# Kernel tuning notes

Measured on AMD Instinct MI355X. Metric: run time of the kernel, lower is better.

The kernel has to match this reference:

```python
import jax, jax.numpy as jnp
import numpy as np

EPS = 1e-5
K_GROUP = 8  # k_group_size


def setup_inputs() -> dict:
    key = jax.random.key(0)
    ks = jax.random.split(key, 8)
    C = 384  # encoder_channel
    rn = lambda k, s: (jax.random.normal(k, s, dtype=jnp.float32) * 0.05)
    return {
        "point_groups": jax.random.normal(ks[0], (4, 256, 32, 3), dtype=jnp.float32),
        # first_conv: Conv1d(3,128,1)+BN+ReLU+Conv1d(128,256,1)
        "W1": rn(ks[1], (128, 3)), "b1": jnp.zeros(128, jnp.float32),
        "gamma1": jnp.ones(128, jnp.float32), "beta1": jnp.zeros(128, jnp.float32),
        "W2": rn(ks[2], (256, 128)), "b2": jnp.zeros(256, jnp.float32),
        # second_conv: Conv1d(512,512,1)+BN+ReLU+Conv1d(512,C,1)
        "W3": rn(ks[3], (512, 512)), "b3": jnp.zeros(512, jnp.float32),
        "gamma3": jnp.ones(512, jnp.float32), "beta3": jnp.zeros(512, jnp.float32),
        "W4": rn(ks[4], (C, 512)), "b4": jnp.zeros(C, jnp.float32),
        # K_Norm affine (out_dim = C, matching declared parameter shapes)
        "alpha": jnp.ones((1, 1, 1, C), jnp.float32),
        "beta_aff": jnp.zeros((1, 1, 1, C), jnp.float32),
        # fusion_layer: Conv1d(2C,C,1)+BN+ReLU
        "Wf": rn(ks[5], (C, 2 * C)), "bf": jnp.zeros(C, jnp.float32),
        "gammaf": jnp.ones(C, jnp.float32), "betaf": jnp.zeros(C, jnp.float32),
    }


def _conv1x1(x, W, b):  # x: (B,Cin,L), W: (Cout,Cin)
    return jnp.einsum("bcl,oc->bol", x, W) + b[None, :, None]


def _bn(x, gamma, beta):  # training-mode BatchNorm1d over (batch, length)
    mu = jnp.mean(x, axis=(0, 2), keepdims=True)
    var = jnp.var(x, axis=(0, 2), keepdims=True)
    xh = (x - mu) * jax.lax.rsqrt(var + EPS)
    return xh * gamma[None, :, None] + beta[None, :, None]


def reference(point_groups, W1, b1, gamma1, beta1, W2, b2, W3, b3, gamma3, beta3,
              W4, b4, alpha, beta_aff, Wf, bf, gammaf, betaf):
    bs, g, n, _ = point_groups.shape
    C = W4.shape[0]
    pg = point_groups.reshape(bs * g, n, 3)  # (B', n, 3)

    # first_conv stack
    f = _conv1x1(pg.transpose(0, 2, 1), W1, b1)           # (B',128,n)
    f = jax.nn.relu(_bn(f, gamma1, beta1))
    f = _conv1x1(f, W2, b2)                               # (B',256,n)
    fg = jnp.max(f, axis=2, keepdims=True)                # (B',256,1)
    f = jnp.concatenate([jnp.broadcast_to(fg, f.shape), f], axis=1)  # (B',512,n)

    # second_conv stack
    f = _conv1x1(f, W3, b3)
    f = jax.nn.relu(_bn(f, gamma3, beta3))
    f = _conv1x1(f, W4, b4)                               # (B',C,n)
    feat = f.transpose(0, 2, 1)                           # (B',n,C)

    # KNN within each group (self included, as in KNN(xyz,xyz))
    sq = jnp.sum(pg * pg, axis=-1)                        # (B',n)
    d = sq[:, :, None] + sq[:, None, :] - 2.0 * jnp.einsum("bnc,bmc->bnm", pg, pg)
    _, idx = jax.lax.top_k(-d, K_GROUP)                   # (B',n,K)

    gather = jax.vmap(lambda a, i: a[i])
    knn_x = gather(feat, idx)                             # (B',n,K,C)

    # K_Norm: center-relative normalization by global scalar std (torch.std, ddof=1)
    mean_x = feat[:, :, None, :]
    dx = knn_x - mean_x
    std_x = jnp.std(dx, ddof=1)
    knn_x = dx / (std_x + EPS)
    knn_x = alpha * knn_x + beta_aff                      # (B',n,K,C)

    enhanced = jnp.mean(knn_x, axis=2)                    # mean over K -> (B',n,C)
    enhanced = jnp.mean(enhanced, axis=1)                 # pool over n -> (B',C)

    fg2 = jnp.max(f, axis=2)                              # (B',C)
    fused_in = jnp.concatenate([fg2, enhanced], axis=1)[:, :, None]  # (B',2C,1)
    fused = jax.nn.relu(_bn(_conv1x1(fused_in, Wf, bf), gammaf, betaf))[:, :, 0]
    return fused.reshape(bs, g, C)
```

## Files before the change

kernel.cpp:

```cpp
#include <hip/hip_runtime.h>
#include <math.h>

#define EPS 1e-5f

typedef __attribute__((ext_vector_type(8))) short s16x8;
typedef __attribute__((ext_vector_type(4))) float f32x4;

__device__ __forceinline__ unsigned short f2bf(float x) {
    unsigned u = __float_as_uint(x);
    u += 0x7fffu + ((u >> 16) & 1u);
    return (unsigned short)(u >> 16);
}
__device__ __forceinline__ float bf2f(unsigned short h) {
    return __uint_as_float(((unsigned)h) << 16);
}
__device__ __forceinline__ unsigned long long pack4bf(float a, float b, float c, float d) {
    return (unsigned long long)f2bf(a)
         | ((unsigned long long)f2bf(b) << 16)
         | ((unsigned long long)f2bf(c) << 32)
         | ((unsigned long long)f2bf(d) << 48);
}

template<int CTRL>
__device__ __forceinline__ float dppmov(float x) {
    return __int_as_float(__builtin_amdgcn_update_dpp(
        0, __float_as_int(x), CTRL, 0xF, 0xF, true));
}
__device__ __forceinline__ float red16_sum(float x) {
    x += dppmov<0xB1>(x);
    x += dppmov<0x4E>(x);
    x += dppmov<0x141>(x);
    x += dppmov<0x140>(x);
    return x;
}
__device__ __forceinline__ float red16_max(float x) {
    x = fmaxf(x, dppmov<0xB1>(x));
    x = fmaxf(x, dppmov<0x4E>(x));
    x = fmaxf(x, dppmov<0x141>(x));
    x = fmaxf(x, dppmov<0x140>(x));
    return x;
}

__global__ __launch_bounds__(128) void k1_prep(
    const float* __restrict__ pg,
    const float* __restrict__ W2, const float* __restrict__ W3,
    const float* __restrict__ W4, const float* __restrict__ Wf,
    float* __restrict__ mom, int* __restrict__ idxw,
    unsigned short* __restrict__ W2b, unsigned short* __restrict__ W3b,
    unsigned short* __restrict__ W4b, unsigned short* __restrict__ Wfb,
    float* __restrict__ p3sb, float* __restrict__ p3qb)
{
    __shared__ float pgs[96];
    __shared__ float sqs[32];
    if (blockIdx.x >= 1024) {
        const int wb = blockIdx.x - 1024;
        const int i = wb * 128 + threadIdx.x;
        if (i < 32768)  W2b[i] = f2bf(W2[i]);
        if (i < 262144) W3b[i] = f2bf(W3[i]);
        if (i < 196608) W4b[i] = f2bf(W4[i]);
        if (i < 294912) Wfb[i] = f2bf(Wf[i]);
        if (wb < 16) {
            for (int j = threadIdx.x; j < 512; j += 128) {
                p3sb[wb*512 + j] = 0.f;
                p3qb[wb*512 + j] = 0.f;
            }
        }
        return;
    }
    const int b = blockIdx.x;
    const int t = threadIdx.x;
    if (t < 96) pgs[t] = pg[b * 96 + t];
    __syncthreads();
    if (t < 32) {
        float x = pgs[t*3+0], y = pgs[t*3+1], z = pgs[t*3+2];
        sqs[t] = x*x + y*y + z*z;
    }
    __syncthreads();
    if (t < 32) {
        const float x = pgs[t*3+0], y = pgs[t*3+1], z = pgs[t*3+2];
        float v[9] = {x, y, z, x*x, x*y, x*z, y*y, y*z, z*z};
        #pragma unroll
        for (int off = 16; off > 0; off >>= 1)
            #pragma unroll
            for (int j = 0; j < 9; ++j)
                v[j] += __shfl_down(v[j], off, 32);
        if (t == 0) {
            #pragma unroll
            for (int j = 0; j < 9; ++j)
                mom[j*1024 + b] = v[j];
        }
        const float sql = sqs[t];
        float dist[32];
        #pragma unroll
        for (int m = 0; m < 32; ++m) {
            float dot = x*pgs[m*3+0] + y*pgs[m*3+1] + z*pgs[m*3+2];
            dist[m] = sql + sqs[m] - 2.f*dot;
        }
        unsigned used = 0u;
        int* orow = idxw + b*256 + t*8;
        #pragma unroll
        for (int j = 0; j < 8; ++j) {
            float best = 3.4e38f; int bi = 0;
            #pragma unroll
            for (int m = 0; m < 32; ++m) {
                if (!((used >> m) & 1u) && dist[m] < best) { best = dist[m]; bi = m; }
            }
            used |= (1u << bi);
            orow[j] = bi;
        }
    }
}

__global__ __launch_bounds__(1024, 8) void k3_mfma(
    const float* __restrict__ pg,
    const float* __restrict__ W1, const float* __restrict__ b1,
    const float* __restrict__ gamma1, const float* __restrict__ beta1,
    const float* __restrict__ mom,
    const unsigned short* __restrict__ W2b, const float* __restrict__ b2,
    const unsigned short* __restrict__ W3b, const float* __restrict__ b3,
    unsigned short* __restrict__ h3b,
    float* __restrict__ p3sb, float* __restrict__ p3qb)
{
    const int g0 = blockIdx.x * 2;
    const int t = threadIdx.x;
    __shared__ __align__(16) unsigned short SB[26128];
    unsigned short* B1  = SB;
    unsigned short* F2  = SB + 8704;
    unsigned short* FGB = SB + 25600;
    __shared__ __align__(16) float sc1s[128], sh1s[128];
    __shared__ __align__(16) float W1s[384], b1s[128];
    __shared__ __align__(16) float pgs3[192];
    __shared__ float momS[9];

    if (t < 192) pgs3[t] = pg[g0*96 + t];
    if (t < 384) W1s[t] = W1[t];
    if (t < 128) b1s[t] = b1[t];
    {
        const int wv = t >> 6, ln = t & 63;
        if (wv < 9) {
            float s = 0.f;
            #pragma unroll
            for (int i = 0; i < 16; ++i)
                s += mom[wv*1024 + ln + 64*i];
            #pragma unroll
            for (int off = 32; off > 0; off >>= 1)
                s += __shfl_down(s, off, 64);
            if (ln == 0) momS[wv] = s;
        }
    }
    __syncthreads();

    if (t < 128) {
        const float Sx = momS[0], Sy = momS[1], Sz = momS[2];
        const float Sxx = momS[3], Sxy = momS[4], Sxz = momS[5];
        const float Syy = momS[6], Syz = momS[7], Szz = momS[8];
        const float w0 = W1s[t*3+0], w1 = W1s[t*3+1], w2 = W1s[t*3+2];
        const float bb = b1s[t];
        const float N = 32768.f;
        const float wd = w0*Sx + w1*Sy + w2*Sz;
        const float S = wd + N*bb;
        const float Q = w0*w0*Sxx + w1*w1*Syy + w2*w2*Szz
                      + 2.f*(w0*w1*Sxy + w0*w2*Sxz + w1*w2*Syz)
                      + 2.f*bb*wd + N*bb*bb;
        const float mu  = S * (1.f/32768.f);
        const float var = Q * (1.f/32768.f) - mu*mu;
        const float sc  = gamma1[t] * rsqrtf(var + EPS);
        sc1s[t] = sc;
        sh1s[t] = beta1[t] - mu * sc;
    }
    __syncthreads();

    {
        const int l = t >> 4, c0 = (t & 15) * 8;
        const float px = pgs3[l*3+0], py = pgs3[l*3+1], pz = pgs3[l*3+2];
        unsigned short ov[8];
        #pragma unroll
        for (int e = 0; e < 8; ++e) {
            const int c = c0 + e;
            float v = fmaf(W1s[c*3+2], pz, fmaf(W1s[c*3+1], py, fmaf(W1s[c*3+0], px, b1s[c])));
            float val = fmaxf(fmaf(v, sc1s[c], sh1s[c]), 0.f);
            ov[e] = f2bf(val);
        }
        uint4 o4;
        o4.x = (unsigned)ov[0] | ((unsigned)ov[1] << 16);
        o4.y = (unsigned)ov[2] | ((unsigned)ov[3] << 16);
        o4.z = (unsigned)ov[4] | ((unsigned)ov[5] << 16);
        o4.w = (unsigned)ov[6] | ((unsigned)ov[7] << 16);
        *(uint4*)&B1[l*136 + c0] = o4;
    }
    __syncthreads();

    const int wave = t >> 6;
    const int lane = t & 63;
    const int m    = lane & 15;
    const int quad = lane >> 4;

    f32x4 acc2[4];
    #pragma unroll
    for (int n = 0; n < 4; ++n)
        acc2[n] = (f32x4){0.f, 0.f, 0.f, 0.f};

    #pragma unroll
    for (int kt = 0; kt < 4; ++kt) {
        s16x8 bv[4];
        #pragma unroll
        for (int nt = 0; nt < 4; ++nt)
            bv[nt] = *(const s16x8*)&B1[(nt*16 + m)*136 + kt*32 + quad*8];
        s16x8 av = *(const s16x8*)(W2b + (size_t)(wave*16 + m)*128 + kt*32 + quad*8);
        #pragma unroll
        for (int nt = 0; nt < 4; ++nt)
            acc2[nt] = __builtin_amdgcn_mfma_f32_16x16x32_bf16(av, bv[nt], acc2[nt], 0, 0, 0);
    }

    {
        const int o0 = wave*16 + quad*4;
        #pragma unroll
        for (int r = 0; r < 4; ++r) {
            float bb = b2[o0 + r];
            #pragma unroll
            for (int nt = 0; nt < 4; ++nt) acc2[nt][r] += bb;
        }
        #pragma unroll
        for (int nt = 0; nt < 4; ++nt) {
            const int row = nt*16 + m;
            *(unsigned long long*)&F2[row*264 + o0] =
                pack4bf(acc2[nt][0], acc2[nt][1], acc2[nt][2], acc2[nt][3]);
        }
        float f0[4], f1[4];
        #pragma unroll
        for (int r = 0; r < 4; ++r) {
            f0[r] = red16_max(fmaxf(acc2[0][r], acc2[1][r]));
            f1[r] = red16_max(fmaxf(acc2[2][r], acc2[3][r]));
        }
        if (m == 0) {
            *(unsigned long long*)&FGB[o0]       = pack4bf(f0[0], f0[1], f0[2], f0[3]);
            *(unsigned long long*)&FGB[264 + o0] = pack4bf(f1[0], f1[1], f1[2], f1[3]);
        }
    }
    __syncthreads();

    unsigned short* dst = h3b + (size_t)blockIdx.x * 32768;
    const int binbase = (blockIdx.x & 15) * 512;
    #pragma unroll
    for (int mt = 0; mt < 2; ++mt) {
        const int ot = wave*2 + mt;
        const int o0 = ot*16 + quad*4;

        f32x4 facc = (f32x4){0.f, 0.f, 0.f, 0.f};
        #pragma unroll
        for (int kt = 0; kt < 8; ++kt) {
            s16x8 bg = *(const s16x8*)&FGB[(m & 1)*264 + kt*32 + quad*8];
            s16x8 av = *(const s16x8*)(W3b + (size_t)(ot*16 + m)*512 + kt*32 + quad*8);
            facc = __builtin_amdgcn_mfma_f32_16x16x32_bf16(av, bg, facc, 0, 0, 0);
        }

        f32x4 acc3[4];
        #pragma unroll
        for (int r = 0; r < 4; ++r) {
            float self = facc[r];
            float oth  = dppmov<0xB1>(self);
            float fg_g0 = (m & 1) ? oth : self;
            float fg_g1 = (m & 1) ? self : oth;
            float bb = b3[o0 + r];
            acc3[0][r] = bb + fg_g0;
            acc3[1][r] = bb + fg_g0;
            acc3[2][r] = bb + fg_g1;
            acc3[3][r] = bb + fg_g1;
        }

        #pragma unroll
        for (int kt = 0; kt < 8; ++kt) {
            s16x8 bv[4];
            #pragma unroll
            for (int nt = 0; nt < 4; ++nt)
                bv[nt] = *(const s16x8*)&F2[(nt*16 + m)*264 + kt*32 + quad*8];
            s16x8 av = *(const s16x8*)(W3b + (size_t)(ot*16 + m)*512 + 256 + kt*32 + quad*8);
            #pragma unroll
            for (int nt = 0; nt < 4; ++nt)
                acc3[nt] = __builtin_amdgcn_mfma_f32_16x16x32_bf16(av, bv[nt], acc3[nt], 0, 0, 0);
        }

        float s[4], q[4];
        #pragma unroll
        for (int r = 0; r < 4; ++r) {
            float x0 = acc3[0][r], x1 = acc3[1][r];
            float x2 = acc3[2][r], x3 = acc3[3][r];
            s[r] = (x0 + x1) + (x2 + x3);
            q[r] = (x0*x0 + x1*x1) + (x2*x2 + x3*x3);
        }
        {
            unsigned long long u0 = pack4bf(acc3[0][0], acc3[0][1], acc3[0][2], acc3[0][3]);
            unsigned long long u1 = pack4bf(acc3[1][0], acc3[1][1], acc3[1][2], acc3[1][3]);
            unsigned long long u2 = pack4bf(acc3[2][0], acc3[2][1], acc3[2][2], acc3[2][3]);
            unsigned long long u3 = pack4bf(acc3[3][0], acc3[3][1], acc3[3][2], acc3[3][3]);
            unsigned short* p = dst + (size_t)(ot*64 + lane) * 16;
            *(uint4*)(p)     = make_uint4((unsigned)u0, (unsigned)(u0 >> 32), (unsigned)u1, (unsigned)(u1 >> 32));
            *(uint4*)(p + 8) = make_uint4((unsigned)u2, (unsigned)(u2 >> 32), (unsigned)u3, (unsigned)(u3 >> 32));
        }
        #pragma unroll
        for (int r = 0; r < 4; ++r) {
            s[r] = red16_sum(s[r]);
            q[r] = red16_sum(q[r]);
        }
        if (m == 0) {
            #pragma unroll
            for (int r = 0; r < 4; ++r) {
                atomicAdd(&p3sb[binbase + o0 + r], s[r]);
                atomicAdd(&p3qb[binbase + o0 + r], q[r]);
            }
        }
    }
}

__global__ __launch_bounds__(768, 6) void k5_mfma(
    const unsigned short* __restrict__ h3b,
    const float* __restrict__ gamma3, const float* __restrict__ beta3,
    const float* __restrict__ p3sb, const float* __restrict__ p3qb,
    const unsigned short* __restrict__ W4b, const float* __restrict__ b4,
    const int* __restrict__ idxw,
    float* __restrict__ fg2, float* __restrict__ A,
    float* __restrict__ S1p, float* __restrict__ S2p)
{
    const int g0 = blockIdx.x * 2;
    const int t = threadIdx.x;
    __shared__ __align__(16) unsigned short SB[33280];
    unsigned short* B4 = SB;
    unsigned short* XT = SB;
    unsigned short* Mm = SB + 30720;
    __shared__ __align__(16) float sc3s[512], sh3s[512];
    __shared__ int icnt[2][32];
    __shared__ float r1[2][12], r2[2][12];

    if (t < 512) {
        float S = 0.f, Q = 0.f;
        #pragma unroll
        for (int bb = 0; bb < 16; ++bb) {
            S += p3sb[bb*512 + t];
            Q += p3qb[bb*512 + t];
        }
        float mu  = S * (1.f/32768.f);
        float var = Q * (1.f/32768.f) - mu*mu;
        float sc  = gamma3[t] * rsqrtf(var + EPS);
        sc3s[t] = sc;
        sh3s[t] = beta3[t] - mu * sc;
    }
    if (t < 64) icnt[t >> 5][t & 31] = 0;
    __syncthreads();

    {
        const uint4* src = (const uint4*)(h3b + (size_t)blockIdx.x * 32768);
        for (int i = t; i < 4096; i += 768) {
            uint4 hv = src[i];
            const int flat16 = i >> 1, half = i & 1;
            const int ln = flat16 & 63, m2 = ln & 15, q2 = ln >> 4;
            const int wm = flat16 >> 6;
            const int o0 = wm*16 + q2*4;
            const float4 sc = *(const float4*)&sc3s[o0];
            const float4 sh = *(const float4*)&sh3s[o0];
            const int rowa = (half*2)*16 + m2;
            float a0 = fmaxf(fmaf(bf2f((unsigned short)(hv.x       )), sc.x, sh.x), 0.f);
            float a1 = fmaxf(fmaf(bf2f((unsigned short)(hv.x >> 16 )), sc.y, sh.y), 0.f);
            float a2 = fmaxf(fmaf(bf2f((unsigned short)(hv.y       )), sc.z, sh.z), 0.f);
            float a3 = fmaxf(fmaf(bf2f((unsigned short)(hv.y >> 16 )), sc.w, sh.w), 0.f);
            float b0 = fmaxf(fmaf(bf2f((unsigned short)(hv.z       )), sc.x, sh.x), 0.f);
            float b1 = fmaxf(fmaf(bf2f((unsigned short)(hv.z >> 16 )), sc.y, sh.y), 0.f);
            float b2 = fmaxf(fmaf(bf2f((unsigned short)(hv.w       )), sc.z, sh.z), 0.f);
            float b3 = fmaxf(fmaf(bf2f((unsigned short)(hv.w >> 16 )), sc.w, sh.w), 0.f);
            *(unsigned long long*)&B4[rowa*520 + o0]        = pack4bf(a0, a1, a2, a3);
            *(unsigned long long*)&B4[(rowa + 16)*520 + o0] = pack4bf(b0, b1, b2, b3);
        }
    }
    __syncthreads();

    const int wave = t >> 6;
    const int lane = t & 63;
    const int m    = lane & 15;
    const int quad = lane >> 4;

    f32x4 acc4[2][4];
    #pragma unroll
    for (int mt = 0; mt < 2; ++mt)
        #pragma unroll
        for (int n = 0; n < 4; ++n)
            acc4[mt][n] = (f32x4){0.f, 0.f, 0.f, 0.f};

    #pragma unroll 4
    for (int kt = 0; kt < 16; ++kt) {
        s16x8 bv[4];
        #pragma unroll
        for (int nt = 0; nt < 4; ++nt)
            bv[nt] = *(const s16x8*)&B4[(nt*16 + m)*520 + kt*32 + quad*8];
        #pragma unroll
        for (int mt = 0; mt < 2; ++mt) {
            s16x8 av = *(const s16x8*)(W4b + (size_t)(wave*32 + mt*16 + m)*512 + kt*32 + quad*8);
            #pragma unroll
            for (int nt = 0; nt < 4; ++nt)
                acc4[mt][nt] = __builtin_amdgcn_mfma_f32_16x16x32_bf16(av, bv[nt], acc4[mt][nt], 0, 0, 0);
        }
    }

    #pragma unroll
    for (int mt = 0; mt < 2; ++mt) {
        const int o0 = wave*32 + mt*16 + quad*4;
        float f0[4], f1[4];
        #pragma unroll
        for (int r = 0; r < 4; ++r) {
            float bb = b4[o0 + r];
            #pragma unroll
            for (int nt = 0; nt < 4; ++nt) acc4[mt][nt][r] += bb;
            f0[r] = red16_max(fmaxf(acc4[mt][0][r], acc4[mt][1][r]));
            f1[r] = red16_max(fmaxf(acc4[mt][2][r], acc4[mt][3][r]));
        }
        if (m == 0) {
            #pragma unroll
            for (int r = 0; r < 4; ++r) {
                fg2[(size_t)g0*384 + o0 + r]     = f0[r];
                fg2[(size_t)(g0+1)*384 + o0 + r] = f1[r];
            }
        }
    }
    __syncthreads();

    #pragma unroll
    for (int mt = 0; mt < 2; ++mt) {
        const int o0 = wave*32 + mt*16 + quad*4;
        #pragma unroll
        for (int nt = 0; nt < 4; ++nt) {
            const int g = nt >> 1;
            const int l = (nt & 1)*16 + m;
            unsigned short* xg = XT + g*15360;
            #pragma unroll
            for (int r = 0; r < 4; ++r)
                xg[(o0 + r)*40 + l] = f2bf(acc4[mt][nt][r]);
        }
    }
    if (t < 64) {
        const int g = t >> 5, l = t & 31;
        uint4 z = make_uint4(0u, 0u, 0u, 0u);
        #pragma unroll
        for (int i = 0; i < 5; ++i)
            *(uint4*)&Mm[g*1280 + l*40 + i*8] = z;
    }
    __syncthreads();

    if (t < 64) {
        const int g = t >> 5, l = t & 31;
        const int* ip = idxw + (size_t)(g0 + g)*256 + l*8;
        #pragma unroll
        for (int j = 0; j < 8; ++j) {
            int ix = ip[j];
            Mm[g*1280 + l*40 + ix] = 0x3F80;
            atomicAdd(&icnt[g][ix], 1);
        }
    }
    __syncthreads();

    float s1loc[2] = {0.f, 0.f}, s2loc[2] = {0.f, 0.f};
    #pragma unroll
    for (int g = 0; g < 2; ++g) {
        const float c0 = (float)icnt[g][m];
        const float c1 = (float)icnt[g][m + 16];
        const float w0 = c0 - 8.f, u0 = c0 + 8.f;
        const float w1 = c1 - 8.f, u1 = c1 + 8.f;
        #pragma unroll
        for (int mt = 0; mt < 2; ++mt) {
            const int o0 = wave*32 + mt*16 + quad*4;
            float Ap[4];
            #pragma unroll
            for (int r = 0; r < 4; ++r) {
                const float x0 = acc4[mt][g*2 + 0][r];
                const float x1 = acc4[mt][g*2 + 1][r];
                Ap[r] = w0*x0 + w1*x1;
                s1loc[g] += Ap[r];
                s2loc[g] += u0*x0*x0 + u1*x1*x1;
            }
            #pragma unroll
            for (int r = 0; r < 4; ++r)
                Ap[r] = red16_sum(Ap[r]);
            if (m == 0) {
                #pragma unroll
                for (int r = 0; r < 4; ++r)
                    A[(size_t)(g0 + g)*384 + o0 + r] = Ap[r];
            }
        }
    }

    #pragma unroll
    for (int g = 0; g < 2; ++g) {
        const unsigned short* xg = XT + g*15360;
        float cross = 0.f;
        #pragma unroll
        for (int lt = 0; lt < 2; ++lt) {
            s16x8 af = *(const s16x8*)&Mm[g*1280 + (lt*16 + m)*40 + quad*8];
            #pragma unroll
            for (int i = 0; i < 2; ++i) {
                const int oc = (wave*2 + i)*16 + m;
                s16x8 bfv = *(const s16x8*)&xg[oc*40 + quad*8];
                f32x4 sa = __builtin_amdgcn_mfma_f32_16x16x32_bf16(
                    af, bfv, (f32x4){0.f, 0.f, 0.f, 0.f}, 0, 0, 0);
                #pragma unroll
                for (int r = 0; r < 4; ++r) {
                    const int lp = lt*16 + quad*4 + r;
                    cross = fmaf(bf2f(xg[oc*40 + lp]), sa[r], cross);
                }
            }
        }
        s2loc[g] -= 2.f * cross;
    }

    #pragma unroll
    for (int g = 0; g < 2; ++g) {
        float sA = s1loc[g], sQ = s2loc[g];
        #pragma unroll
        for (int off = 32; off > 0; off >>= 1) {
            sA += __shfl_down(sA, off, 64);
            sQ += __shfl_down(sQ, off, 64);
        }
        if (lane == 0) { r1[g][wave] = sA; r2[g][wave] = sQ; }
    }
    __syncthreads();
    if (t < 2) {
        float S = 0.f, Q = 0.f;
        #pragma unroll
        for (int w = 0; w < 12; ++w) { S += r1[t][w]; Q += r2[t][w]; }
        S1p[g0 + t] = S;
        S2p[g0 + t] = Q;
    }
}

__global__ __launch_bounds__(384) void k7_fused(
    const float* __restrict__ fg2, const float* __restrict__ A,
    const float* __restrict__ alpha, const float* __restrict__ beta_aff,
    const float* __restrict__ S1p, const float* __restrict__ S2p,
    const unsigned short* __restrict__ Wfb, const float* __restrict__ bf,
    float* __restrict__ hf, float* __restrict__ pfs, float* __restrict__ pfq)
{
    const int blk    = blockIdx.x;
    const int slice  = blk >> 2;
    const int msplit = blk & 3;
    const int g0     = slice * 16;
    const int obase  = msplit * 96;
    const int t = threadIdx.x;
    __shared__ __align__(16) char smem[24832];
    unsigned short* xfb = (unsigned short*)smem;
    float* OTf = (float*)smem;
    __shared__ double rs[6], rq[6];
    __shared__ float stdsh;

    {
        double s = 0.0, q = 0.0;
        for (int i = t; i < 1024; i += 384) { s += (double)S1p[i]; q += (double)S2p[i]; }
        #pragma unroll
        for (int off = 32; off > 0; off >>= 1) {
            s += __shfl_down(s, off, 64);
            q += __shfl_down(q, off, 64);
        }
        if ((t & 63) == 0) { rs[t >> 6] = s; rq[t >> 6] = q; }
        __syncthreads();
        if (t == 0) {
            double S = 0.0, Q = 0.0;
            #pragma unroll
            for (int w = 0; w < 6; ++w) { S += rs[w]; Q += rq[w]; }
            const double N = 1024.0 * 32.0 * 8.0 * 384.0;
            double var = (Q - S*S/N) / (N - 1.0);
            stdsh = (float)sqrt(var);
        }
        __syncthreads();
    }
    const float inv = 1.f / (256.f * (stdsh + EPS));

    for (int i = t; i < 16*96; i += 384) {
        const int row = i / 96, c8 = (i % 96) * 8;
        const int g = g0 + row;
        float e[8];
        if (c8 < 384) {
            const float4* s0 = (const float4*)(fg2 + (size_t)g*384 + c8);
            float4 v0 = s0[0], v1 = s0[1];
            e[0]=v0.x; e[1]=v0.y; e[2]=v0.z; e[3]=v0.w;
            e[4]=v1.x; e[5]=v1.y; e[6]=v1.z; e[7]=v1.w;
        } else {
            const int cc = c8 - 384;
            const float4* s0 = (const float4*)(A + (size_t)g*384 + cc);
            float4 v0 = s0[0], v1 = s0[1];
            float av[8] = {v0.x,v0.y,v0.z,v0.w,v1.x,v1.y,v1.z,v1.w};
            #pragma unroll
            for (int j = 0; j < 8; ++j)
                e[j] = fmaf(alpha[cc+j] * inv, av[j], beta_aff[cc+j]);
        }
        uint4 o4;
        o4.x = (unsigned)f2bf(e[0]) | ((unsigned)f2bf(e[1]) << 16);
        o4.y = (unsigned)f2bf(e[2]) | ((unsigned)f2bf(e[3]) << 16);
        o4.z = (unsigned)f2bf(e[4]) | ((unsigned)f2bf(e[5]) << 16);
        o4.w = (unsigned)f2bf(e[6]) | ((unsigned)f2bf(e[7]) << 16);
        *(uint4*)&xfb[row*776 + c8] = o4;
    }
    __syncthreads();

    const int wave = t >> 6;
    const int lane = t & 63;
    const int m    = lane & 15;
    const int quad = lane >> 4;

    f32x4 acc = (f32x4){0.f, 0.f, 0.f, 0.f};
    #pragma unroll 4
    for (int kt = 0; kt < 24; ++kt) {
        s16x8 bv = *(const s16x8*)&xfb[m*776 + kt*32 + quad*8];
        s16x8 av = *(const s16x8*)(Wfb + (size_t)(obase + wave*16 + m)*768 + kt*32 + quad*8);
        acc = __builtin_amdgcn_mfma_f32_16x16x32_bf16(av, bv, acc, 0, 0, 0);
    }

    {
        const int o0 = obase + wave*16 + quad*4;
        float s[4], q[4];
        #pragma unroll
        for (int r = 0; r < 4; ++r) {
            acc[r] += bf[o0 + r];
            s[r] = red16_sum(acc[r]);
            q[r] = red16_sum(acc[r]*acc[r]);
        }
        if (m == 0) {
            #pragma unroll
            for (int r = 0; r < 4; ++r) {
                pfs[(size_t)slice*384 + o0 + r] = s[r];
                pfq[(size_t)slice*384 + o0 + r] = q[r];
            }
        }
    }
    __syncthreads();

    {
        const int lo0 = wave*16 + quad*4;
        #pragma unroll
        for (int r = 0; r < 4; ++r)
            OTf[m*100 + lo0 + r] = acc[r];
    }
    __syncthreads();

    {
        const int grp = t / 24, c4 = t % 24;
        float4 v = *(const float4*)&OTf[grp*100 + c4*4];
        *(float4*)(hf + (size_t)(g0 + grp)*384 + obase + c4*4) = v;
    }
}

__global__ __launch_bounds__(384) void k9_out(
    const float* __restrict__ hf,
    const float* __restrict__ pfs, const float* __restrict__ pfq,
    const float* __restrict__ gammaf, const float* __restrict__ betaf,
    float* __restrict__ out)
{
    const int blk = blockIdx.x, t = threadIdx.x;
    float S = 0.f, Q = 0.f;
    #pragma unroll 8
    for (int i = 0; i < 64; ++i) {
        S += pfs[(size_t)i*384 + t];
        Q += pfq[(size_t)i*384 + t];
    }
    const float mu  = S * (1.f/1024.f);
    const float var = Q * (1.f/1024.f) - mu*mu;
    const float sc  = gammaf[t] * rsqrtf(var + EPS);
    const float sh  = betaf[t] - mu * sc;
    const size_t base = (size_t)blk * 8 * 384;
    #pragma unroll
    for (int g = 0; g < 8; ++g) {
        float v = fmaf(hf[base + g*384 + t], sc, sh);
        out[base + g*384 + t] = fmaxf(v, 0.f);
    }
}

extern "C" void kernel_launch(void* const* d_in, const int* in_sizes, int n_in,
                              void* d_out, int out_size, void* d_ws, size_t ws_size,
                              hipStream_t stream) {
    const float* pg      = (const float*)d_in[0];
    const float* W1      = (const float*)d_in[1];
    const float* b1      = (const float*)d_in[2];
    const float* gamma1  = (const float*)d_in[3];
    const float* beta1   = (const float*)d_in[4];
    const float* W2      = (const float*)d_in[5];
    const float* b2      = (const float*)d_in[6];
    const float* W3      = (const float*)d_in[7];
    const float* b3      = (const float*)d_in[8];
    const float* gamma3  = (const float*)d_in[9];
    const float* beta3   = (const float*)d_in[10];
    const float* W4      = (const float*)d_in[11];
    const float* b4      = (const float*)d_in[12];
    const float* alpha   = (const float*)d_in[13];
    const float* beta_af = (const float*)d_in[14];
    const float* Wf      = (const float*)d_in[15];
    const float* bf      = (const float*)d_in[16];
    const float* gammaf  = (const float*)d_in[17];
    const float* betaf   = (const float*)d_in[18];
    float* out = (float*)d_out;

    float* w = (float*)d_ws;
    unsigned short* h3b = (unsigned short*)w; w += 1024*16384/2;
    unsigned short* W2b = (unsigned short*)w; w += 32768/2;
    unsigned short* W3b = (unsigned short*)w; w += 262144/2;
    unsigned short* W4b = (unsigned short*)w; w += 196608/2;
    unsigned short* Wfb = (unsigned short*)w; w += 294912/2;
    float* hf     = w;  w += 1024*384;
    float* fg2    = w;  w += 1024*384;
    float* A      = w;  w += 1024*384;
    float* mom    = w;  w += 12*1024;
    float* p3sb   = w;  w += 16*512;
    float* p3qb   = w;  w += 16*512;
    float* pfs    = w;  w += 64*384;
    float* pfq    = w;  w += 64*384;
    float* S1p    = w;  w += 1024;
    float* S2p    = w;  w += 1024;
    int*   idxw   = (int*)w;  w += 1024*256;

    hipLaunchKernelGGL(k1_prep, dim3(1024 + 2304), dim3(128), 0, stream,
                       pg, W2, W3, W4, Wf,
                       mom, idxw, W2b, W3b, W4b, Wfb, p3sb, p3qb);
    hipLaunchKernelGGL(k3_mfma, dim3(512), dim3(1024), 0, stream,
                       pg, W1, b1, gamma1, beta1, mom, W2b, b2, W3b, b3,
                       h3b, p3sb, p3qb);
    hipLaunchKernelGGL(k5_mfma, dim3(512), dim3(768), 0, stream,
                       h3b, gamma3, beta3, p3sb, p3qb, W4b, b4, idxw,
                       fg2, A, S1p, S2p);
    hipLaunchKernelGGL(k7_fused, dim3(256), dim3(384), 0, stream,
                       fg2, A, alpha, beta_af, S1p, S2p, Wfb, bf, hf, pfs, pfq);
    hipLaunchKernelGGL(k9_out, dim3(128), dim3(384), 0, stream,
                       hf, pfs, pfq, gammaf, betaf, out);
}
```

Measured before the change: 194.2 us.

## Fuse conv3 and conv4 kernels with a grid-wide atomic barrier

Merges the W3 GEMM kernel and the W4/KNN kernel into one launch. A global atomic counter acts as a grid barrier, so the block waits until all BN3 partial statistics are accumulated and then continues straight into the second stage. This removes one kernel launch and the gap between the two kernels. In exchange it needs all 512 blocks to be co-resident to avoid deadlock, leaves four of the sixteen waves idle in the second phase, and raises LDS use to the larger of the two kernels.

```diff
diff --git a/kernel.cpp b/kernel.cpp
--- a/kernel.cpp
+++ b/kernel.cpp
@@ -48,7 +48,8 @@
     float* __restrict__ mom, int* __restrict__ idxw,
     unsigned short* __restrict__ W2b, unsigned short* __restrict__ W3b,
     unsigned short* __restrict__ W4b, unsigned short* __restrict__ Wfb,
-    float* __restrict__ p3sb, float* __restrict__ p3qb)
+    float* __restrict__ p3sb, float* __restrict__ p3qb,
+    unsigned* __restrict__ barcnt)
 {
     __shared__ float pgs[96];
     __shared__ float sqs[32];
@@ -65,6 +66,7 @@
                 p3qb[wb*512 + j] = 0.f;
             }
         }
+        if (wb == 16 && threadIdx.x < 2) barcnt[threadIdx.x] = 0u;
         return;
     }
     const int b = blockIdx.x;
@@ -111,26 +113,38 @@
     }
 }
 
-__global__ __launch_bounds__(1024, 8) void k3_mfma(
+__global__ __launch_bounds__(1024, 8) void k35_fused(
     const float* __restrict__ pg,
     const float* __restrict__ W1, const float* __restrict__ b1,
     const float* __restrict__ gamma1, const float* __restrict__ beta1,
     const float* __restrict__ mom,
     const unsigned short* __restrict__ W2b, const float* __restrict__ b2,
     const unsigned short* __restrict__ W3b, const float* __restrict__ b3,
+    const float* __restrict__ gamma3, const float* __restrict__ beta3,
+    const unsigned short* __restrict__ W4b, const float* __restrict__ b4,
+    const int* __restrict__ idxw,
     unsigned short* __restrict__ h3b,
-    float* __restrict__ p3sb, float* __restrict__ p3qb)
+    float* __restrict__ p3sb, float* __restrict__ p3qb,
+    unsigned* __restrict__ barcnt,
+    float* __restrict__ fg2, float* __restrict__ A,
+    float* __restrict__ S1p, float* __restrict__ S2p)
 {
     const int g0 = blockIdx.x * 2;
     const int t = threadIdx.x;
-    __shared__ __align__(16) unsigned short SB[26128];
+    __shared__ __align__(16) unsigned short SB[33280];
     unsigned short* B1  = SB;
     unsigned short* F2  = SB + 8704;
     unsigned short* FGB = SB + 25600;
+    unsigned short* B4  = SB;
+    unsigned short* XT  = SB;
+    unsigned short* Mm  = SB + 30720;
     __shared__ __align__(16) float sc1s[128], sh1s[128];
     __shared__ __align__(16) float W1s[384], b1s[128];
     __shared__ __align__(16) float pgs3[192];
     __shared__ float momS[9];
+    __shared__ __align__(16) float sc3s[512], sh3s[512];
+    __shared__ int icnt[2][32];
+    __shared__ float r1[2][12], r2[2][12];
 
     if (t < 192) pgs3[t] = pg[g0*96 + t];
     if (t < 384) W1s[t] = W1[t];
@@ -310,33 +324,21 @@
             }
         }
     }
-}
-
-__global__ __launch_bounds__(768, 6) void k5_mfma(
-    const unsigned short* __restrict__ h3b,
-    const float* __restrict__ gamma3, const float* __restrict__ beta3,
-    const float* __restrict__ p3sb, const float* __restrict__ p3qb,
-    const unsigned short* __restrict__ W4b, const float* __restrict__ b4,
-    const int* __restrict__ idxw,
-    float* __restrict__ fg2, float* __restrict__ A,
-    float* __restrict__ S1p, float* __restrict__ S2p)
-{
-    const int g0 = blockIdx.x * 2;
-    const int t = threadIdx.x;
-    __shared__ __align__(16) unsigned short SB[33280];
-    unsigned short* B4 = SB;
-    unsigned short* XT = SB;
-    unsigned short* Mm = SB + 30720;
-    __shared__ __align__(16) float sc3s[512], sh3s[512];
-    __shared__ int icnt[2][32];
-    __shared__ float r1[2][12], r2[2][12];
+
+    __syncthreads();
+    if (t == 0) {
+        __hip_atomic_fetch_add(&barcnt[0], 1u, __ATOMIC_ACQ_REL, __HIP_MEMORY_SCOPE_AGENT);
+        while (__hip_atomic_load(&barcnt[0], __ATOMIC_ACQUIRE, __HIP_MEMORY_SCOPE_AGENT) < 512u)
+            __builtin_amdgcn_s_sleep(8);
+    }
+    __syncthreads();
 
     if (t < 512) {
         float S = 0.f, Q = 0.f;
         #pragma unroll
         for (int bb = 0; bb < 16; ++bb) {
-            S += p3sb[bb*512 + t];
-            Q += p3qb[bb*512 + t];
+            S += __hip_atomic_load(&p3sb[bb*512 + t], __ATOMIC_RELAXED, __HIP_MEMORY_SCOPE_AGENT);
+            Q += __hip_atomic_load(&p3qb[bb*512 + t], __ATOMIC_RELAXED, __HIP_MEMORY_SCOPE_AGENT);
         }
         float mu  = S * (1.f/32768.f);
         float var = Q * (1.f/32768.f) - mu*mu;
@@ -349,7 +351,7 @@
 
     {
         const uint4* src = (const uint4*)(h3b + (size_t)blockIdx.x * 32768);
-        for (int i = t; i < 4096; i += 768) {
+        for (int i = t; i < 4096; i += 1024) {
             uint4 hv = src[i];
             const int flat16 = i >> 1, half = i & 1;
             const int ln = flat16 & 63, m2 = ln & 15, q2 = ln >> 4;
@@ -372,11 +374,6 @@
     }
     __syncthreads();
 
-    const int wave = t >> 6;
-    const int lane = t & 63;
-    const int m    = lane & 15;
-    const int quad = lane >> 4;
-
     f32x4 acc4[2][4];
     #pragma unroll
     for (int mt = 0; mt < 2; ++mt)
@@ -384,54 +381,58 @@
         for (int n = 0; n < 4; ++n)
             acc4[mt][n] = (f32x4){0.f, 0.f, 0.f, 0.f};
 
-    #pragma unroll 4
-    for (int kt = 0; kt < 16; ++kt) {
-        s16x8 bv[4];
-        #pragma unroll
-        for (int nt = 0; nt < 4; ++nt)
-            bv[nt] = *(const s16x8*)&B4[(nt*16 + m)*520 + kt*32 + quad*8];
+    if (wave < 12) {
+        #pragma unroll 4
+        for (int kt = 0; kt < 16; ++kt) {
+            s16x8 bv[4];
+            #pragma unroll
+            for (int nt = 0; nt < 4; ++nt)
+                bv[nt] = *(const s16x8*)&B4[(nt*16 + m)*520 + kt*32 + quad*8];
+            #pragma unroll
+            for (int mt = 0; mt < 2; ++mt) {
+                s16x8 av = *(const s16x8*)(W4b + (size_t)(wave*32 + mt*16 + m)*512 + kt*32 + quad*8);
+                #pragma unroll
+                for (int nt = 0; nt < 4; ++nt)
+                    acc4[mt][nt] = __builtin_amdgcn_mfma_f32_16x16x32_bf16(av, bv[nt], acc4[mt][nt], 0, 0, 0);
+            }
+        }
+
         #pragma unroll
         for (int mt = 0; mt < 2; ++mt) {
-            s16x8 av = *(const s16x8*)(W4b + (size_t)(wave*32 + mt*16 + m)*512 + kt*32 + quad*8);
-            #pragma unroll
-            for (int nt = 0; nt < 4; ++nt)
-                acc4[mt][nt] = __builtin_amdgcn_mfma_f32_16x16x32_bf16(av, bv[nt], acc4[mt][nt], 0, 0, 0);
-        }
-    }
-
-    #pragma unroll
-    for (int mt = 0; mt < 2; ++mt) {
-        const int o0 = wave*32 + mt*16 + quad*4;
-        float f0[4], f1[4];
-        #pragma unroll
-        for (int r = 0; r < 4; ++r) {
-            float bb = b4[o0 + r];
-            #pragma unroll
-            for (int nt = 0; nt < 4; ++nt) acc4[mt][nt][r] += bb;
-            f0[r] = red16_max(fmaxf(acc4[mt][0][r], acc4[mt][1][r]));
-            f1[r] = red16_max(fmaxf(acc4[mt][2][r], acc4[mt][3][r]));
-        }
-        if (m == 0) {
+            const int o0 = wave*32 + mt*16 + quad*4;
+            float f0[4], f1[4];
             #pragma unroll
             for (int r = 0; r < 4; ++r) {
-                fg2[(size_t)g0*384 + o0 + r]     = f0[r];
-                fg2[(size_t)(g0+1)*384 + o0 + r] = f1[r];
-            }
-        }
-    }
-    __syncthreads();
-
-    #pragma unroll
-    for (int mt = 0; mt < 2; ++mt) {
-        const int o0 = wave*32 + mt*16 + quad*4;
-        #pragma unroll
-        for (int nt = 0; nt < 4; ++nt) {
-            const int g = nt >> 1;
-            const int l = (nt & 1)*16 + m;
-            unsigned short* xg = XT + g*15360;
-            #pragma unroll
-            for (int r = 0; r < 4; ++r)
-                xg[(o0 + r)*40 + l] = f2bf(acc4[mt][nt][r]);
+                float bb = b4[o0 + r];
+                #pragma unroll
+                for (int nt = 0; nt < 4; ++nt) acc4[mt][nt][r] += bb;
+                f0[r] = red16_max(fmaxf(acc4[mt][0][r], acc4[mt][1][r]));
+                f1[r] = red16_max(fmaxf(acc4[mt][2][r], acc4[mt][3][r]));
+            }
+            if (m == 0) {
+                #pragma unroll
+                for (int r = 0; r < 4; ++r) {
+                    fg2[(size_t)g0*384 + o0 + r]     = f0[r];
+                    fg2[(size_t)(g0+1)*384 + o0 + r] = f1[r];
+                }
+            }
+        }
+    }
+    __syncthreads();
+
+    if (wave < 12) {
+        #pragma unroll
+        for (int mt = 0; mt < 2; ++mt) {
+            const int o0 = wave*32 + mt*16 + quad*4;
+            #pragma unroll
+            for (int nt = 0; nt < 4; ++nt) {
+                const int g = nt >> 1;
+                const int l = (nt & 1)*16 + m;
+                unsigned short* xg = XT + g*15360;
+                #pragma unroll
+                for (int r = 0; r < 4; ++r)
+                    xg[(o0 + r)*40 + l] = f2bf(acc4[mt][nt][r]);
+            }
         }
     }
     if (t < 64) {
@@ -456,56 +457,58 @@
     __syncthreads();
 
     float s1loc[2] = {0.f, 0.f}, s2loc[2] = {0.f, 0.f};
-    #pragma unroll
-    for (int g = 0; g < 2; ++g) {
-        const float c0 = (float)icnt[g][m];
-        const float c1 = (float)icnt[g][m + 16];
-        const float w0 = c0 - 8.f, u0 = c0 + 8.f;
-        const float w1 = c1 - 8.f, u1 = c1 + 8.f;
-        #pragma unroll
-        for (int mt = 0; mt < 2; ++mt) {
-            const int o0 = wave*32 + mt*16 + quad*4;
-            float Ap[4];
-            #pragma unroll
-            for (int r = 0; r < 4; ++r) {
-                const float x0 = acc4[mt][g*2 + 0][r];
-                const float x1 = acc4[mt][g*2 + 1][r];
-                Ap[r] = w0*x0 + w1*x1;
-                s1loc[g] += Ap[r];
-                s2loc[g] += u0*x0*x0 + u1*x1*x1;
-            }
-            #pragma unroll
-            for (int r = 0; r < 4; ++r)
-                Ap[r] = red16_sum(Ap[r]);
-            if (m == 0) {
+    if (wave < 12) {
+        #pragma unroll
+        for (int g = 0; g < 2; ++g) {
+            const float c0 = (float)icnt[g][m];
+            const float c1 = (float)icnt[g][m + 16];
+            const float w0 = c0 - 8.f, u0 = c0 + 8.f;
+            const float w1 = c1 - 8.f, u1 = c1 + 8.f;
+            #pragma unroll
+            for (int mt = 0; mt < 2; ++mt) {
+                const int o0 = wave*32 + mt*16 + quad*4;
+                float Ap[4];
+                #pragma unroll
+                for (int r = 0; r < 4; ++r) {
+                    const float x0 = acc4[mt][g*2 + 0][r];
+                    const float x1 = acc4[mt][g*2 + 1][r];
+                    Ap[r] = w0*x0 + w1*x1;
+                    s1loc[g] += Ap[r];
+                    s2loc[g] += u0*x0*x0 + u1*x1*x1;
+                }
                 #pragma unroll
                 for (int r = 0; r < 4; ++r)
-                    A[(size_t)(g0 + g)*384 + o0 + r] = Ap[r];
-            }
-        }
-    }
-
-    #pragma unroll
-    for (int g = 0; g < 2; ++g) {
-        const unsigned short* xg = XT + g*15360;
-        float cross = 0.f;
-        #pragma unroll
-        for (int lt = 0; lt < 2; ++lt) {
-            s16x8 af = *(const s16x8*)&Mm[g*1280 + (lt*16 + m)*40 + quad*8];
-            #pragma unroll
-            for (int i = 0; i < 2; ++i) {
-                const int oc = (wave*2 + i)*16 + m;
-                s16x8 bfv = *(const s16x8*)&xg[oc*40 + quad*8];
-                f32x4 sa = __builtin_amdgcn_mfma_f32_16x16x32_bf16(
-                    af, bfv, (f32x4){0.f, 0.f, 0.f, 0.f}, 0, 0, 0);
+                    Ap[r] = red16_sum(Ap[r]);
+                if (m == 0) {
+                    #pragma unroll
+                    for (int r = 0; r < 4; ++r)
+                        A[(size_t)(g0 + g)*384 + o0 + r] = Ap[r];
+                }
+            }
+        }
+
+        #pragma unroll
+        for (int g = 0; g < 2; ++g) {
+            const unsigned short* xg = XT + g*15360;
+            float cross = 0.f;
+            #pragma unroll
+            for (int lt = 0; lt < 2; ++lt) {
+                s16x8 af = *(const s16x8*)&Mm[g*1280 + (lt*16 + m)*40 + quad*8];
                 #pragma unroll
-                for (int r = 0; r < 4; ++r) {
-                    const int lp = lt*16 + quad*4 + r;
-                    cross = fmaf(bf2f(xg[oc*40 + lp]), sa[r], cross);
+                for (int i = 0; i < 2; ++i) {
+                    const int oc = (wave*2 + i)*16 + m;
+                    s16x8 bfv = *(const s16x8*)&xg[oc*40 + quad*8];
+                    f32x4 sa = __builtin_amdgcn_mfma_f32_16x16x32_bf16(
+                        af, bfv, (f32x4){0.f, 0.f, 0.f, 0.f}, 0, 0, 0);
+                    #pragma unroll
+                    for (int r = 0; r < 4; ++r) {
+                        const int lp = lt*16 + quad*4 + r;
+                        cross = fmaf(bf2f(xg[oc*40 + lp]), sa[r], cross);
+                    }
                 }
             }
-        }
-        s2loc[g] -= 2.f * cross;
+            s2loc[g] -= 2.f * cross;
+        }
     }
 
     #pragma unroll
@@ -516,7 +519,7 @@
             sA += __shfl_down(sA, off, 64);
             sQ += __shfl_down(sQ, off, 64);
         }
-        if (lane == 0) { r1[g][wave] = sA; r2[g][wave] = sQ; }
+        if (lane == 0 && wave < 12) { r1[g][wave] = sA; r2[g][wave] = sQ; }
     }
     __syncthreads();
     if (t < 2) {
@@ -709,16 +712,15 @@
     float* S1p    = w;  w += 1024;
     float* S2p    = w;  w += 1024;
     int*   idxw   = (int*)w;  w += 1024*256;
+    unsigned* barcnt = (unsigned*)w; w += 2;
 
     hipLaunchKernelGGL(k1_prep, dim3(1024 + 2304), dim3(128), 0, stream,
                        pg, W2, W3, W4, Wf,
-                       mom, idxw, W2b, W3b, W4b, Wfb, p3sb, p3qb);
-    hipLaunchKernelGGL(k3_mfma, dim3(512), dim3(1024), 0, stream,
+                       mom, idxw, W2b, W3b, W4b, Wfb, p3sb, p3qb, barcnt);
+    hipLaunchKernelGGL(k35_fused, dim3(512), dim3(1024), 0, stream,
                        pg, W1, b1, gamma1, beta1, mom, W2b, b2, W3b, b3,
-                       h3b, p3sb, p3qb);
-    hipLaunchKernelGGL(k5_mfma, dim3(512), dim3(768), 0, stream,
-                       h3b, gamma3, beta3, p3sb, p3qb, W4b, b4, idxw,
-                       fg2, A, S1p, S2p);
+                       gamma3, beta3, W4b, b4, idxw,
+                       h3b, p3sb, p3qb, barcnt, fg2, A, S1p, S2p);
     hipLaunchKernelGGL(k7_fused, dim3(256), dim3(384), 0, stream,
                        fg2, A, alpha, beta_af, S1p, S2p, Wfb, bf, hf, pfs, pfq);
     hipLaunchKernelGGL(k9_out, dim3(128), dim3(384), 0, stream,
```

Result: slower. 317.7 us (+63.6%).
